# Performance work log

Hardware: AMD Instinct MI355X
Metric: run time of the kernel (lower is better)

Reference implementation:

```python
import jax, jax.numpy as jnp
import numpy as np

B, N, DIM = 8, 4096, 128

def setup_inputs() -> dict:
    key = jax.random.key(0)
    ks = jax.random.split(key, 6)
    s = 1.0 / np.sqrt(DIM)
    return {
        "x": jax.random.normal(ks[0], (B, N, DIM), dtype=jnp.float32),
        "q_global": jax.random.normal(ks[1], (B, N, DIM), dtype=jnp.float32),
        "Wkv": jax.random.normal(ks[2], (DIM, 2 * DIM), dtype=jnp.float32) * s,
        "bkv": jax.random.normal(ks[3], (2 * DIM,), dtype=jnp.float32) * 0.02,
        "Wp": jax.random.normal(ks[4], (DIM, DIM), dtype=jnp.float32) * s,
        "bp": jax.random.normal(ks[5], (DIM,), dtype=jnp.float32) * 0.02,
    }

def reference(x, q_global, Wkv, bkv, Wp, bp):
    # x: [B, n, dim]; kv linear -> split into k, v (each [B, n, dim])
    kv = x @ Wkv + bkv
    k, v = jnp.split(kv, 2, axis=-1)
    dim = x.shape[-1]
    q = q_global * (1.0 / jnp.sqrt(jnp.asarray(dim, x.dtype)))
    # scores = k @ q^T : [B, n, m]; softmax over query axis m (as in source)
    scores = jnp.einsum("bnd,bmd->bnm", k, q)
    attn = jax.nn.softmax(scores, axis=-1)
    # attention @ v : contracts m against v's row index (m == n)
    out = jnp.einsum("bnm,bmd->bnd", attn, v)
    return out @ Wp + bp
```

## Files before the change

### kernel.cpp

```cpp
#include <hip/hip_runtime.h>

typedef __bf16 bf16x8 __attribute__((ext_vector_type(8)));
typedef float f32x4 __attribute__((ext_vector_type(4)));
typedef float f32x16 __attribute__((ext_vector_type(16)));

struct alignas(16) US8 { unsigned short us[8]; };

static __device__ inline unsigned short f2bf(float f) {
  union { float f; unsigned u; } v; v.f = f;
  unsigned r = v.u + 0x7fffu + ((v.u >> 16) & 1u);
  return (unsigned short)(r >> 16);
}

static __device__ inline void gload16(const unsigned short* g, unsigned short* l) {
  __builtin_amdgcn_global_load_lds(
      (const __attribute__((address_space(1))) void*)g,
      (__attribute__((address_space(3))) void*)l, 16, 0, 0);
}

#define NSEQ 4096
#define DIM 128
#define ROWS 32768
#define KH 4

#define EXPC (1.4426950408889634f * 0.08838834764831845f)

__global__ void prep_kernel(const float* __restrict__ Wkv, const float* __restrict__ Wp,
                            unsigned short* __restrict__ wkvT, unsigned short* __restrict__ wpT) {
  const int t = threadIdx.x;
  const int d = (t & 63) * 2;
  if (blockIdx.x < 64) {
    const int col = blockIdx.x * 4 + (t >> 6);
    unsigned short lo = f2bf(Wkv[d * 256 + col]);
    unsigned short hi = f2bf(Wkv[(d + 1) * 256 + col]);
    *reinterpret_cast<unsigned*>(&wkvT[col * 128 + d]) = (unsigned)lo | ((unsigned)hi << 16);
  } else {
    const int col = (blockIdx.x - 64) * 4 + (t >> 6);
    unsigned short lo = f2bf(Wp[d * 128 + col]);
    unsigned short hi = f2bf(Wp[(d + 1) * 128 + col]);
    *reinterpret_cast<unsigned*>(&wpT[col * 128 + d]) = (unsigned)lo | ((unsigned)hi << 16);
  }
}

__global__ __launch_bounds__(256, 4) void kvq_kernel(
    const float* __restrict__ x, const unsigned short* __restrict__ wkvT,
    const float* __restrict__ bkv, const float* __restrict__ q,
    unsigned short* __restrict__ kout, unsigned short* __restrict__ vtout,
    unsigned short* __restrict__ qo) {
  const int tid = threadIdx.x;
  __shared__ __align__(16) unsigned short WT[128 * 136];
  if (blockIdx.x >= 1024) {
    int i = ((blockIdx.x - 1024) * 256 + tid) * 8;
    const float4* p = reinterpret_cast<const float4*>(q + i);
    float4 a = p[0], b = p[1];
    US8 o;
    o.us[0]=f2bf(a.x*EXPC); o.us[1]=f2bf(a.y*EXPC); o.us[2]=f2bf(a.z*EXPC); o.us[3]=f2bf(a.w*EXPC);
    o.us[4]=f2bf(b.x*EXPC); o.us[5]=f2bf(b.y*EXPC); o.us[6]=f2bf(b.z*EXPC); o.us[7]=f2bf(b.w*EXPC);
    int row = i >> 7, d0 = i & 127;
    int bb = row >> 12, n = row & (NSEQ - 1), tile = n >> 6, l = n & 63, kc = d0 >> 3;
    *reinterpret_cast<US8*>(qo + (size_t)bb * NSEQ * DIM + tile * 8192 + kc * 512 + l * 8) = o;
    return;
  }
  const int wv = tid >> 6, lane = tid & 63, l16 = lane & 15, quad = lane >> 4;
  const int half = blockIdx.x & 1;
  const int row0 = (blockIdx.x >> 1) * 64;

  for (int p = 0; p < 8; ++p) {
    int c = p * 256 + tid;
    int col = c >> 4, c16 = c & 15;
    *reinterpret_cast<US8*>(&WT[col * 136 + c16 * 8]) =
        *reinterpret_cast<const US8*>(wkvT + (half * 128 + col) * 128 + c16 * 8);
  }
  __syncthreads();

  bf16x8 afrag[4];
  const int arow = row0 + wv * 16 + l16;
  for (int s = 0; s < 4; ++s) {
    const float4* xp = reinterpret_cast<const float4*>(x + (size_t)arow * DIM + s * 32 + quad * 8);
    float4 u0 = xp[0], u1 = xp[1];
    US8 af;
    af.us[0]=f2bf(u0.x); af.us[1]=f2bf(u0.y); af.us[2]=f2bf(u0.z); af.us[3]=f2bf(u0.w);
    af.us[4]=f2bf(u1.x); af.us[5]=f2bf(u1.y); af.us[6]=f2bf(u1.z); af.us[7]=f2bf(u1.w);
    afrag[s] = __builtin_bit_cast(bf16x8, af);
  }
  f32x4 acc[8];
  for (int g = 0; g < 8; ++g) acc[g] = f32x4{0.f, 0.f, 0.f, 0.f};
  for (int s = 0; s < 4; ++s)
    for (int g = 0; g < 8; ++g) {
      bf16x8 bfr = *reinterpret_cast<const bf16x8*>(&WT[(g * 16 + l16) * 136 + s * 32 + quad * 8]);
      acc[g] = __builtin_amdgcn_mfma_f32_16x16x32_bf16(afrag[s], bfr, acc[g], 0, 0, 0);
    }

  __syncthreads();
  if (half == 0) {
    for (int g = 0; g < 8; ++g) {
      float bias = bkv[g * 16 + l16];
      for (int r = 0; r < 4; ++r)
        WT[(wv * 16 + quad * 4 + r) * 136 + g * 16 + l16] = f2bf(acc[g][r] + bias);
    }
    __syncthreads();
    unsigned short* kbo = kout + (size_t)row0 * DIM;
    for (int p = 0; p < 4; ++p) {
      int c = p * 256 + tid;
      int rowl = c >> 4, seg = c & 15;
      *reinterpret_cast<uint4*>(kbo + (size_t)rowl * DIM + seg * 8) =
          *reinterpret_cast<const uint4*>(&WT[rowl * 136 + seg * 8]);
    }
  } else {
    unsigned short* LDSt = WT;
    for (int g = 0; g < 8; ++g) {
      float bias = bkv[128 + g * 16 + l16];
      for (int r = 0; r < 4; ++r)
        LDSt[(g * 16 + l16) * 72 + wv * 16 + quad * 4 + r] = f2bf(acc[g][r] + bias);
    }
    __syncthreads();
    const int bb = row0 >> 12;
    const int tile = (row0 & (NSEQ - 1)) >> 6;
    unsigned short* vbo = vtout + (size_t)bb * NSEQ * DIM + (size_t)tile * 8192;
    for (int p = 0; p < 4; ++p) {
      int c = p * 256 + tid;
      int idx = c >> 6, l = c & 63;
      int mg = idx >> 1, dh = idx & 1, d = dh * 64 + l;
      int nb = (mg >> 1) * 16 + (mg & 1) * 4;
      uint2 lo = *reinterpret_cast<const uint2*>(&LDSt[d * 72 + nb]);
      uint2 hi = *reinterpret_cast<const uint2*>(&LDSt[d * 72 + nb + 8]);
      uint4 o{lo.x, lo.y, hi.x, hi.y};
      *reinterpret_cast<uint4*>(vbo + (size_t)idx * 512 + l * 8) = o;
    }
  }
}

__global__ __launch_bounds__(256, 2) void attn_kernel(
    const unsigned short* __restrict__ kbuf, const unsigned short* __restrict__ qblk,
    const unsigned short* __restrict__ vblk,
    unsigned short* __restrict__ opart, float* __restrict__ lpart) {
  __shared__ __align__(16) unsigned short SH[32768];
  const int tid = threadIdx.x;
  const int wv = tid >> 6, lane = tid & 63, l32 = lane & 31, h = lane >> 5;
  const int b = blockIdx.x & 7;
  const int t = blockIdx.x >> 3;
  const int q0 = (t & 15) * 256;
  const int kh = t >> 4;
  const int key0 = kh * (NSEQ / KH);
  const unsigned short* kb = kbuf + (size_t)b * NSEQ * DIM;
  const unsigned short* qb = qblk + (size_t)b * NSEQ * DIM;
  const unsigned short* vb = vblk + (size_t)b * NSEQ * DIM;

  const unsigned short* sbase = ((wv < 2) ? qb : vb) + (size_t)(key0 >> 6) * 8192
                                + (wv & 1) * 4096 + lane * 8;
  const int ldst = (wv >> 1) * 8192 + (wv & 1) * 4096;

  constexpr int NT = NSEQ / KH / 64;

#pragma unroll
  for (int c = 0; c < 8; ++c)
    gload16(sbase + c * 512, &SH[ldst + c * 512]);

  bf16x8 kfrag[2][8];
#pragma unroll
  for (int nf = 0; nf < 2; ++nf)
#pragma unroll
    for (int ks = 0; ks < 8; ++ks)
      kfrag[nf][ks] = __builtin_bit_cast(bf16x8, *reinterpret_cast<const US8*>(
          kb + (size_t)(q0 + nf * 128 + wv * 32 + l32) * DIM + ks * 16 + h * 8));

  f32x16 Oacc[2][4];
#pragma unroll
  for (int nf = 0; nf < 2; ++nf)
    for (int dt = 0; dt < 4; ++dt)
      for (int i = 0; i < 16; ++i) Oacc[nf][dt][i] = 0.f;
  float lsum0 = 0.f, lsum1 = 0.f;

  __syncthreads();

  for (int it = 0; it < NT; ++it) {
    const int cur = (it & 1) << 14;
    if (it + 1 < NT) {
      const int nxt = cur ^ 16384;
      const unsigned short* sp = sbase + (size_t)(it + 1) * 8192;
#pragma unroll
      for (int c = 0; c < 8; ++c)
        gload16(sp + c * 512, &SH[nxt + ldst + c * 512]);
    }
    const unsigned short* Qsh = SH + cur;
    const unsigned short* Vsh = Qsh + 8192;

#pragma unroll
    for (int T = 0; T < 2; ++T) {
      bf16x8 pA[2], pB[2];
      {
        f32x16 S;
        for (int i = 0; i < 16; ++i) S[i] = 0.f;
        __builtin_amdgcn_s_setprio(1);
#pragma unroll
        for (int ks = 0; ks < 8; ++ks) {
          bf16x8 a = *reinterpret_cast<const bf16x8*>(
              &Qsh[(ks * 2 + h) * 512 + (T * 32 + l32) * 8]);
          S = __builtin_amdgcn_mfma_f32_32x32x16_bf16(a, kfrag[0][ks], S, 0, 0, 0);
        }
        __builtin_amdgcn_s_setprio(0);
        unsigned pk[8];
#pragma unroll
        for (int i2 = 0; i2 < 8; ++i2) {
          float e0 = __builtin_amdgcn_exp2f(S[i2 * 2]);
          float e1 = __builtin_amdgcn_exp2f(S[i2 * 2 + 1]);
          lsum0 += e0; lsum0 += e1;
          pk[i2] = __builtin_amdgcn_perm(__builtin_bit_cast(unsigned, e1),
                                         __builtin_bit_cast(unsigned, e0), 0x07060302u);
        }
        pA[0] = __builtin_bit_cast(bf16x8, uint4{pk[0], pk[1], pk[2], pk[3]});
        pA[1] = __builtin_bit_cast(bf16x8, uint4{pk[4], pk[5], pk[6], pk[7]});
      }
      {
        f32x16 S;
        for (int i = 0; i < 16; ++i) S[i] = 0.f;
        __builtin_amdgcn_s_setprio(1);
#pragma unroll
        for (int ks = 0; ks < 8; ++ks) {
          bf16x8 a = *reinterpret_cast<const bf16x8*>(
              &Qsh[(ks * 2 + h) * 512 + (T * 32 + l32) * 8]);
          S = __builtin_amdgcn_mfma_f32_32x32x16_bf16(a, kfrag[1][ks], S, 0, 0, 0);
        }
        __builtin_amdgcn_s_setprio(0);
        unsigned pk[8];
#pragma unroll
        for (int i2 = 0; i2 < 8; ++i2) {
          float e0 = __builtin_amdgcn_exp2f(S[i2 * 2]);
          float e1 = __builtin_amdgcn_exp2f(S[i2 * 2 + 1]);
          lsum1 += e0; lsum1 += e1;
          pk[i2] = __builtin_amdgcn_perm(__builtin_bit_cast(unsigned, e1),
                                         __builtin_bit_cast(unsigned, e0), 0x07060302u);
        }
        pB[0] = __builtin_bit_cast(bf16x8, uint4{pk[0], pk[1], pk[2], pk[3]});
        pB[1] = __builtin_bit_cast(bf16x8, uint4{pk[4], pk[5], pk[6], pk[7]});
      }
      __builtin_amdgcn_s_setprio(1);
#pragma unroll
      for (int s = 0; s < 2; ++s) {
        const int mg = 4 * T + 2 * s + h;
#pragma unroll
        for (int dt = 0; dt < 4; ++dt) {
          bf16x8 bv = *reinterpret_cast<const bf16x8*>(
              &Vsh[(mg * 2 + (dt >> 1)) * 512 + ((dt & 1) * 32 + l32) * 8]);
          Oacc[0][dt] = __builtin_amdgcn_mfma_f32_32x32x16_bf16(pA[s], bv, Oacc[0][dt], 0, 0, 0);
          Oacc[1][dt] = __builtin_amdgcn_mfma_f32_32x32x16_bf16(pB[s], bv, Oacc[1][dt], 0, 0, 0);
        }
      }
      __builtin_amdgcn_s_setprio(0);
    }

    __syncthreads();
  }

  {
    float v0 = lsum0 + __shfl_xor(lsum0, 32);
    float v1 = lsum1 + __shfl_xor(lsum1, 32);
    if (lane < 32) {
      lpart[(size_t)kh * ROWS + (size_t)b * NSEQ + q0 + wv * 32 + l32] = v0;
      lpart[(size_t)kh * ROWS + (size_t)b * NSEQ + q0 + 128 + wv * 32 + l32] = v1;
    }
  }
#pragma unroll
  for (int nf = 0; nf < 2; ++nf) {
    unsigned short* ob = opart + (size_t)kh * ROWS * DIM
                         + ((size_t)b * NSEQ + q0 + nf * 128 + wv * 32) * DIM;
    for (int dt = 0; dt < 4; ++dt)
      for (int i = 0; i < 16; ++i) {
        int n = (i & 3) + 8 * (i >> 2) + 4 * h;
        ob[n * DIM + dt * 32 + l32] = f2bf(Oacc[nf][dt][i]);
      }
  }
}

__global__ __launch_bounds__(256, 4) void combine_proj_kernel(
    const unsigned short* __restrict__ opart, const float* __restrict__ lpart,
    const unsigned short* __restrict__ wpT, const float* __restrict__ bp,
    float* __restrict__ out) {
  __shared__ __align__(16) unsigned short WT[128 * 136];
  const int tid = threadIdx.x;
  const int wv = tid >> 6, lane = tid & 63, l16 = lane & 15, quad = lane >> 4;
  const int row0 = blockIdx.x * 64;

  for (int p = 0; p < 8; ++p) {
    int c = p * 256 + tid;
    int col = c >> 4, c16 = c & 15;
    *reinterpret_cast<US8*>(&WT[col * 136 + c16 * 8]) =
        *reinterpret_cast<const US8*>(wpT + col * 128 + c16 * 8);
  }
  __syncthreads();

  f32x4 acc[8];
  for (int g = 0; g < 8; ++g) acc[g] = f32x4{0.f, 0.f, 0.f, 0.f};
  const int arow = row0 + wv * 16 + l16;
  float lsum = 0.f;
#pragma unroll
  for (int p = 0; p < KH; ++p) lsum += lpart[(size_t)p * ROWS + arow];
  float linv = 1.f / lsum;
  for (int s = 0; s < 4; ++s) {
    const size_t base = (size_t)arow * DIM + s * 32 + quad * 8;
    float f[8] = {0.f, 0.f, 0.f, 0.f, 0.f, 0.f, 0.f, 0.f};
#pragma unroll
    for (int p = 0; p < KH; ++p) {
      US8 u = *reinterpret_cast<const US8*>(opart + (size_t)p * ROWS * DIM + base);
#pragma unroll
      for (int j = 0; j < 8; ++j)
        f[j] += __builtin_bit_cast(float, (unsigned)u.us[j] << 16);
    }
    US8 af;
#pragma unroll
    for (int j = 0; j < 8; ++j) af.us[j] = f2bf(f[j] * linv);
    bf16x8 a = __builtin_bit_cast(bf16x8, af);
    for (int g = 0; g < 8; ++g) {
      bf16x8 bfr = *reinterpret_cast<const bf16x8*>(&WT[(g * 16 + l16) * 136 + s * 32 + quad * 8]);
      acc[g] = __builtin_amdgcn_mfma_f32_16x16x32_bf16(a, bfr, acc[g], 0, 0, 0);
    }
  }
  for (int g = 0; g < 8; ++g) {
    float bias = bp[g * 16 + l16];
    for (int r = 0; r < 4; ++r) {
      int orow = row0 + wv * 16 + quad * 4 + r;
      out[(size_t)orow * DIM + g * 16 + l16] = acc[g][r] + bias;
    }
  }
}

extern "C" void kernel_launch(void* const* d_in, const int* in_sizes, int n_in,
                              void* d_out, int out_size, void* d_ws, size_t ws_size,
                              hipStream_t stream) {
  (void)in_sizes; (void)n_in; (void)out_size; (void)ws_size;
  const float* x   = (const float*)d_in[0];
  const float* qg  = (const float*)d_in[1];
  const float* Wkv = (const float*)d_in[2];
  const float* bkv = (const float*)d_in[3];
  const float* Wp  = (const float*)d_in[4];
  const float* bp  = (const float*)d_in[5];
  float* out = (float*)d_out;

  unsigned short* qbf  = (unsigned short*)d_ws;
  unsigned short* kbf  = qbf + (size_t)ROWS * DIM;
  unsigned short* vtbf = kbf + (size_t)ROWS * DIM;
  unsigned short* wkvT = vtbf + (size_t)ROWS * DIM;
  unsigned short* wpT  = wkvT + 256 * 128;
  float* lpart = (float*)(wpT + 128 * 128);
  unsigned short* opart = (unsigned short*)(lpart + (size_t)KH * ROWS);

  hipLaunchKernelGGL(prep_kernel, dim3(96), dim3(256), 0, stream, Wkv, Wp, wkvT, wpT);
  hipLaunchKernelGGL(kvq_kernel, dim3(1024 + 2048), dim3(256), 0, stream,
                     x, wkvT, bkv, qg, kbf, vtbf, qbf);
  hipLaunchKernelGGL(attn_kernel, dim3(8 * 16 * KH), dim3(256), 0, stream, kbf, qbf, vtbf, opart, lpart);
  hipLaunchKernelGGL(combine_proj_kernel, dim3(ROWS / 64), dim3(256), 0, stream, opart, lpart, wpT, bp, out);
}
```

Measured before the change: 165.8 us.

## Fuse weight prep and combine-projection into neighbouring kernels via grid barrier

Removes the separate weight-transpose kernel by converting and transposing the fp32 Wkv/Wp tiles directly into LDS inside the consumer kernels. Merges the combine+projection kernel into the attention kernel behind a software grid-wide barrier (atomic counter with spin-wait), which saves two launches. It also splits the QK MFMA accumulation into two independent chains to shorten dependency latency. The grid barrier relies on all 512 blocks being co-resident. Each block now re-reads and transposes the fp32 weights with strided scalar LDS writes.

```diff
diff --git a/kernel.cpp b/kernel.cpp
--- a/kernel.cpp
+++ b/kernel.cpp
@@ -22,32 +22,17 @@
 #define DIM 128
 #define ROWS 32768
 #define KH 4
+#define NBLK 512
 
 #define EXPC (1.4426950408889634f * 0.08838834764831845f)
 
-__global__ void prep_kernel(const float* __restrict__ Wkv, const float* __restrict__ Wp,
-                            unsigned short* __restrict__ wkvT, unsigned short* __restrict__ wpT) {
-  const int t = threadIdx.x;
-  const int d = (t & 63) * 2;
-  if (blockIdx.x < 64) {
-    const int col = blockIdx.x * 4 + (t >> 6);
-    unsigned short lo = f2bf(Wkv[d * 256 + col]);
-    unsigned short hi = f2bf(Wkv[(d + 1) * 256 + col]);
-    *reinterpret_cast<unsigned*>(&wkvT[col * 128 + d]) = (unsigned)lo | ((unsigned)hi << 16);
-  } else {
-    const int col = (blockIdx.x - 64) * 4 + (t >> 6);
-    unsigned short lo = f2bf(Wp[d * 128 + col]);
-    unsigned short hi = f2bf(Wp[(d + 1) * 128 + col]);
-    *reinterpret_cast<unsigned*>(&wpT[col * 128 + d]) = (unsigned)lo | ((unsigned)hi << 16);
-  }
-}
-
 __global__ __launch_bounds__(256, 4) void kvq_kernel(
-    const float* __restrict__ x, const unsigned short* __restrict__ wkvT,
+    const float* __restrict__ x, const float* __restrict__ Wkv,
     const float* __restrict__ bkv, const float* __restrict__ q,
     unsigned short* __restrict__ kout, unsigned short* __restrict__ vtout,
-    unsigned short* __restrict__ qo) {
+    unsigned short* __restrict__ qo, int* cnt) {
   const int tid = threadIdx.x;
+  if (blockIdx.x == 0 && tid == 0) *cnt = 0;
   __shared__ __align__(16) unsigned short WT[128 * 136];
   if (blockIdx.x >= 1024) {
     int i = ((blockIdx.x - 1024) * 256 + tid) * 8;
@@ -65,11 +50,12 @@
   const int half = blockIdx.x & 1;
   const int row0 = (blockIdx.x >> 1) * 64;
 
-  for (int p = 0; p < 8; ++p) {
+  for (int p = 0; p < 32; ++p) {
     int c = p * 256 + tid;
-    int col = c >> 4, c16 = c & 15;
-    *reinterpret_cast<US8*>(&WT[col * 136 + c16 * 8]) =
-        *reinterpret_cast<const US8*>(wkvT + (half * 128 + col) * 128 + c16 * 8);
+    int col0 = (c & 63) * 2, d = c >> 6;
+    float2 w = *reinterpret_cast<const float2*>(Wkv + d * 256 + half * 128 + col0);
+    WT[col0 * 136 + d] = f2bf(w.x);
+    WT[(col0 + 1) * 136 + d] = f2bf(w.y);
   }
   __syncthreads();
 
@@ -133,7 +119,9 @@
 __global__ __launch_bounds__(256, 2) void attn_kernel(
     const unsigned short* __restrict__ kbuf, const unsigned short* __restrict__ qblk,
     const unsigned short* __restrict__ vblk,
-    unsigned short* __restrict__ opart, float* __restrict__ lpart) {
+    unsigned short* __restrict__ opart, float* __restrict__ lpart,
+    const float* __restrict__ Wp, const float* __restrict__ bp,
+    float* __restrict__ out, int* cnt) {
   __shared__ __align__(16) unsigned short SH[32768];
   const int tid = threadIdx.x;
   const int wv = tid >> 6, lane = tid & 63, l32 = lane & 31, h = lane >> 5;
@@ -189,21 +177,26 @@
     for (int T = 0; T < 2; ++T) {
       bf16x8 pA[2], pB[2];
       {
-        f32x16 S;
-        for (int i = 0; i < 16; ++i) S[i] = 0.f;
+        f32x16 Se, So;
+        for (int i = 0; i < 16; ++i) { Se[i] = 0.f; So[i] = 0.f; }
         __builtin_amdgcn_s_setprio(1);
 #pragma unroll
-        for (int ks = 0; ks < 8; ++ks) {
-          bf16x8 a = *reinterpret_cast<const bf16x8*>(
+        for (int ks = 0; ks < 8; ks += 2) {
+          bf16x8 a0 = *reinterpret_cast<const bf16x8*>(
               &Qsh[(ks * 2 + h) * 512 + (T * 32 + l32) * 8]);
-          S = __builtin_amdgcn_mfma_f32_32x32x16_bf16(a, kfrag[0][ks], S, 0, 0, 0);
+          bf16x8 a1 = *reinterpret_cast<const bf16x8*>(
+              &Qsh[((ks + 1) * 2 + h) * 512 + (T * 32 + l32) * 8]);
+          Se = __builtin_amdgcn_mfma_f32_32x32x16_bf16(a0, kfrag[0][ks], Se, 0, 0, 0);
+          So = __builtin_amdgcn_mfma_f32_32x32x16_bf16(a1, kfrag[0][ks + 1], So, 0, 0, 0);
         }
         __builtin_amdgcn_s_setprio(0);
+#pragma unroll
+        for (int i = 0; i < 16; ++i) Se[i] += So[i];
         unsigned pk[8];
 #pragma unroll
         for (int i2 = 0; i2 < 8; ++i2) {
-          float e0 = __builtin_amdgcn_exp2f(S[i2 * 2]);
-          float e1 = __builtin_amdgcn_exp2f(S[i2 * 2 + 1]);
+          float e0 = __builtin_amdgcn_exp2f(Se[i2 * 2]);
+          float e1 = __builtin_amdgcn_exp2f(Se[i2 * 2 + 1]);
           lsum0 += e0; lsum0 += e1;
           pk[i2] = __builtin_amdgcn_perm(__builtin_bit_cast(unsigned, e1),
                                          __builtin_bit_cast(unsigned, e0), 0x07060302u);
@@ -212,21 +205,26 @@
         pA[1] = __builtin_bit_cast(bf16x8, uint4{pk[4], pk[5], pk[6], pk[7]});
       }
       {
-        f32x16 S;
-        for (int i = 0; i < 16; ++i) S[i] = 0.f;
+        f32x16 Se, So;
+        for (int i = 0; i < 16; ++i) { Se[i] = 0.f; So[i] = 0.f; }
         __builtin_amdgcn_s_setprio(1);
 #pragma unroll
-        for (int ks = 0; ks < 8; ++ks) {
-          bf16x8 a = *reinterpret_cast<const bf16x8*>(
+        for (int ks = 0; ks < 8; ks += 2) {
+          bf16x8 a0 = *reinterpret_cast<const bf16x8*>(
               &Qsh[(ks * 2 + h) * 512 + (T * 32 + l32) * 8]);
-          S = __builtin_amdgcn_mfma_f32_32x32x16_bf16(a, kfrag[1][ks], S, 0, 0, 0);
+          bf16x8 a1 = *reinterpret_cast<const bf16x8*>(
+              &Qsh[((ks + 1) * 2 + h) * 512 + (T * 32 + l32) * 8]);
+          Se = __builtin_amdgcn_mfma_f32_32x32x16_bf16(a0, kfrag[1][ks], Se, 0, 0, 0);
+          So = __builtin_amdgcn_mfma_f32_32x32x16_bf16(a1, kfrag[1][ks + 1], So, 0, 0, 0);
         }
         __builtin_amdgcn_s_setprio(0);
+#pragma unroll
+        for (int i = 0; i < 16; ++i) Se[i] += So[i];
         unsigned pk[8];
 #pragma unroll
         for (int i2 = 0; i2 < 8; ++i2) {
-          float e0 = __builtin_amdgcn_exp2f(S[i2 * 2]);
-          float e1 = __builtin_amdgcn_exp2f(S[i2 * 2 + 1]);
+          float e0 = __builtin_amdgcn_exp2f(Se[i2 * 2]);
+          float e1 = __builtin_amdgcn_exp2f(Se[i2 * 2 + 1]);
           lsum1 += e0; lsum1 += e1;
           pk[i2] = __builtin_amdgcn_perm(__builtin_bit_cast(unsigned, e1),
                                          __builtin_bit_cast(unsigned, e0), 0x07060302u);
@@ -270,56 +268,62 @@
         ob[n * DIM + dt * 32 + l32] = f2bf(Oacc[nf][dt][i]);
       }
   }
-}
-
-__global__ __launch_bounds__(256, 4) void combine_proj_kernel(
-    const unsigned short* __restrict__ opart, const float* __restrict__ lpart,
-    const unsigned short* __restrict__ wpT, const float* __restrict__ bp,
-    float* __restrict__ out) {
-  __shared__ __align__(16) unsigned short WT[128 * 136];
-  const int tid = threadIdx.x;
-  const int wv = tid >> 6, lane = tid & 63, l16 = lane & 15, quad = lane >> 4;
-  const int row0 = blockIdx.x * 64;
-
-  for (int p = 0; p < 8; ++p) {
-    int c = p * 256 + tid;
-    int col = c >> 4, c16 = c & 15;
-    *reinterpret_cast<US8*>(&WT[col * 136 + c16 * 8]) =
-        *reinterpret_cast<const US8*>(wpT + col * 128 + c16 * 8);
-  }
-  __syncthreads();
-
-  f32x4 acc[8];
-  for (int g = 0; g < 8; ++g) acc[g] = f32x4{0.f, 0.f, 0.f, 0.f};
-  const int arow = row0 + wv * 16 + l16;
-  float lsum = 0.f;
-#pragma unroll
-  for (int p = 0; p < KH; ++p) lsum += lpart[(size_t)p * ROWS + arow];
-  float linv = 1.f / lsum;
-  for (int s = 0; s < 4; ++s) {
-    const size_t base = (size_t)arow * DIM + s * 32 + quad * 8;
-    float f[8] = {0.f, 0.f, 0.f, 0.f, 0.f, 0.f, 0.f, 0.f};
-#pragma unroll
-    for (int p = 0; p < KH; ++p) {
-      US8 u = *reinterpret_cast<const US8*>(opart + (size_t)p * ROWS * DIM + base);
-#pragma unroll
-      for (int j = 0; j < 8; ++j)
-        f[j] += __builtin_bit_cast(float, (unsigned)u.us[j] << 16);
-    }
-    US8 af;
-#pragma unroll
-    for (int j = 0; j < 8; ++j) af.us[j] = f2bf(f[j] * linv);
-    bf16x8 a = __builtin_bit_cast(bf16x8, af);
+
+  __threadfence();
+  __syncthreads();
+  if (tid == 0) {
+    atomicAdd(cnt, 1);
+    while (__hip_atomic_load(cnt, __ATOMIC_ACQUIRE, __HIP_MEMORY_SCOPE_AGENT) < NBLK)
+      __builtin_amdgcn_s_sleep(2);
+    __threadfence();
+  }
+  __syncthreads();
+
+  {
+    unsigned short* WT = SH;
+    for (int p = 0; p < 32; ++p) {
+      int c = p * 256 + tid;
+      int col0 = (c & 63) * 2, d = c >> 6;
+      float2 w = *reinterpret_cast<const float2*>(Wp + d * 128 + col0);
+      WT[col0 * 136 + d] = f2bf(w.x);
+      WT[(col0 + 1) * 136 + d] = f2bf(w.y);
+    }
+    __syncthreads();
+
+    const int l16 = lane & 15, quad = lane >> 4;
+    const int row0c = (int)blockIdx.x * 64;
+    f32x4 acc[8];
+    for (int g = 0; g < 8; ++g) acc[g] = f32x4{0.f, 0.f, 0.f, 0.f};
+    const int arow = row0c + wv * 16 + l16;
+    float lsum = 0.f;
+#pragma unroll
+    for (int p = 0; p < KH; ++p) lsum += lpart[(size_t)p * ROWS + arow];
+    float linv = 1.f / lsum;
+    for (int s = 0; s < 4; ++s) {
+      const size_t base = (size_t)arow * DIM + s * 32 + quad * 8;
+      float f[8] = {0.f, 0.f, 0.f, 0.f, 0.f, 0.f, 0.f, 0.f};
+#pragma unroll
+      for (int p = 0; p < KH; ++p) {
+        US8 u = *reinterpret_cast<const US8*>(opart + (size_t)p * ROWS * DIM + base);
+#pragma unroll
+        for (int j = 0; j < 8; ++j)
+          f[j] += __builtin_bit_cast(float, (unsigned)u.us[j] << 16);
+      }
+      US8 af;
+#pragma unroll
+      for (int j = 0; j < 8; ++j) af.us[j] = f2bf(f[j] * linv);
+      bf16x8 a = __builtin_bit_cast(bf16x8, af);
+      for (int g = 0; g < 8; ++g) {
+        bf16x8 bfr = *reinterpret_cast<const bf16x8*>(&WT[(g * 16 + l16) * 136 + s * 32 + quad * 8]);
+        acc[g] = __builtin_amdgcn_mfma_f32_16x16x32_bf16(a, bfr, acc[g], 0, 0, 0);
+      }
+    }
     for (int g = 0; g < 8; ++g) {
-      bf16x8 bfr = *reinterpret_cast<const bf16x8*>(&WT[(g * 16 + l16) * 136 + s * 32 + quad * 8]);
-      acc[g] = __builtin_amdgcn_mfma_f32_16x16x32_bf16(a, bfr, acc[g], 0, 0, 0);
-    }
-  }
-  for (int g = 0; g < 8; ++g) {
-    float bias = bp[g * 16 + l16];
-    for (int r = 0; r < 4; ++r) {
-      int orow = row0 + wv * 16 + quad * 4 + r;
-      out[(size_t)orow * DIM + g * 16 + l16] = acc[g][r] + bias;
+      float bias = bp[g * 16 + l16];
+      for (int r = 0; r < 4; ++r) {
+        int orow = row0c + wv * 16 + quad * 4 + r;
+        out[(size_t)orow * DIM + g * 16 + l16] = acc[g][r] + bias;
+      }
     }
   }
 }
@@ -339,14 +343,12 @@
   unsigned short* qbf  = (unsigned short*)d_ws;
   unsigned short* kbf  = qbf + (size_t)ROWS * DIM;
   unsigned short* vtbf = kbf + (size_t)ROWS * DIM;
-  unsigned short* wkvT = vtbf + (size_t)ROWS * DIM;
-  unsigned short* wpT  = wkvT + 256 * 128;
-  float* lpart = (float*)(wpT + 128 * 128);
+  float* lpart = (float*)(vtbf + (size_t)ROWS * DIM);
   unsigned short* opart = (unsigned short*)(lpart + (size_t)KH * ROWS);
-
-  hipLaunchKernelGGL(prep_kernel, dim3(96), dim3(256), 0, stream, Wkv, Wp, wkvT, wpT);
+  int* cnt = (int*)(opart + (size_t)KH * ROWS * DIM);
+
   hipLaunchKernelGGL(kvq_kernel, dim3(1024 + 2048), dim3(256), 0, stream,
-                     x, wkvT, bkv, qg, kbf, vtbf, qbf);
-  hipLaunchKernelGGL(attn_kernel, dim3(8 * 16 * KH), dim3(256), 0, stream, kbf, qbf, vtbf, opart, lpart);
-  hipLaunchKernelGGL(combine_proj_kernel, dim3(ROWS / 64), dim3(256), 0, stream, opart, lpart, wpT, bp, out);
-}
+                     x, Wkv, bkv, qg, kbf, vtbf, qbf, cnt);
+  hipLaunchKernelGGL(attn_kernel, dim3(NBLK), dim3(256), 0, stream,
+                     kbf, qbf, vtbf, opart, lpart, Wp, bp, out, cnt);
+}
```

Measured after the change: 315.9 us. 90.5% more time.
